# Kernel tuning notes

Hardware: AMD Instinct MI355X
Metric: run time of the kernel (lower is better)

Reference implementation:

```python
import jax, jax.numpy as jnp
import numpy as np

B, T, C, H = 2, 4096, 768, 12
D = C // H  # head_dim = 64


def setup_inputs() -> dict:
    key = jax.random.key(0)
    k1, k2, k3 = jax.random.split(key, 3)
    x = jax.random.normal(k1, (B, T, C), dtype=jnp.float32)
    w_qkv = jax.random.normal(k2, (C, 3 * C), dtype=jnp.float32) * (1.0 / np.sqrt(C))
    w_out = jax.random.normal(k3, (C, C), dtype=jnp.float32) * (1.0 / np.sqrt(C))
    return {"x": x, "w_qkv": w_qkv, "w_out": w_out}


def reference(x, w_qkv, w_out):
    b, t, c = x.shape
    qkv = x @ w_qkv                              # (B,T,3C)
    q, k, v = jnp.split(qkv, 3, axis=-1)
    # (B,T,C) -> (B,H,T,D)
    q = q.reshape(b, t, H, D).transpose(0, 2, 1, 3)
    k = k.reshape(b, t, H, D).transpose(0, 2, 1, 3)
    v = v.reshape(b, t, H, D).transpose(0, 2, 1, 3)
    att = jnp.einsum('bhqd,bhkd->bhqk', q, k) / jnp.sqrt(jnp.float32(D))
    causal = jnp.tril(jnp.ones((t, t), dtype=bool))  # True where allowed
    att = jnp.where(causal, att, -jnp.inf)
    att = jax.nn.softmax(att, axis=-1)
    y = jnp.einsum('bhqk,bhkd->bhqd', att, v)        # (B,H,T,D)
    y = y.transpose(0, 2, 1, 3).reshape(b, t, c)
    return y @ w_out
```

## Files before the change

kernel.cpp:

```cpp
#include <hip/hip_runtime.h>
#include <stdint.h>
#include <stddef.h>

#define NB 2
#define NT 4096
#define NC 768
#define NH 12
#define ND 64

typedef unsigned short u16;
typedef __attribute__((ext_vector_type(2))) float f32x2;
typedef __attribute__((ext_vector_type(4))) float f32x4;
typedef __attribute__((ext_vector_type(16))) float f32x16;
typedef __attribute__((ext_vector_type(8))) unsigned short u16x8;
typedef __attribute__((ext_vector_type(4))) unsigned short u16x4;
typedef __attribute__((ext_vector_type(8))) __bf16 bf16x8;
typedef __attribute__((ext_vector_type(4))) unsigned int u32x4;

typedef __attribute__((address_space(1))) const unsigned int gu32;
typedef __attribute__((address_space(3))) unsigned int lu32;

__device__ __forceinline__ u16 f2bf(float f) {
  uint32_t u = __builtin_bit_cast(uint32_t, f);
  u += 0x7FFFu + ((u >> 16) & 1u);
  return (u16)(u >> 16);
}
__device__ __forceinline__ bf16x8 asbf(u16x8 v) { return __builtin_bit_cast(bf16x8, v); }

__device__ __forceinline__ uint32_t pkbf(float a, float b) {
  uint32_t ua = __builtin_bit_cast(uint32_t, a) + 0x8000u;
  uint32_t ub = __builtin_bit_cast(uint32_t, b) + 0x8000u;
  return __builtin_amdgcn_perm(ub, ua, 0x07060302u);
}
__device__ __forceinline__ uint32_t pktr(float a, float b) {
  return __builtin_amdgcn_perm(__builtin_bit_cast(uint32_t, b),
                               __builtin_bit_cast(uint32_t, a), 0x07060302u);
}

#define GLDS(gsrc, ldst) __builtin_amdgcn_global_load_lds( \
    (gu32*)(gsrc), (lu32*)(ldst), 16, 0, 0)

#define PRE_CAST_BLKS 6144
#define PRE_TA_BX 72
#define PRE_TA_BLKS (72 * 24)
#define PRE_TB_BX 24
#define PRE_TB_BLKS (24 * 24)
__global__ __launch_bounds__(256)
void k_pre(const float* __restrict__ x, u16* __restrict__ xb,
           const float* __restrict__ w_qkv, u16* __restrict__ wqT,
           const float* __restrict__ w_out, u16* __restrict__ woT) {
  __shared__ float tile[32][33];
  const int bid = blockIdx.x;
  const int tid = threadIdx.x;
  if (bid < PRE_CAST_BLKS) {
    int i = bid * 256 + tid;
    f32x4 v = ((const f32x4*)x)[i];
    u16x4 o;
    o[0] = f2bf(v[0]); o[1] = f2bf(v[1]); o[2] = f2bf(v[2]); o[3] = f2bf(v[3]);
    ((u16x4*)xb)[i] = o;
    return;
  }
  const float* in;
  u16* out;
  int R, Cn, bx, by;
  if (bid < PRE_CAST_BLKS + PRE_TA_BLKS) {
    int q = bid - PRE_CAST_BLKS;
    bx = q % PRE_TA_BX; by = q / PRE_TA_BX;
    in = w_qkv; out = wqT; R = NC; Cn = 3 * NC;
  } else {
    int q = bid - PRE_CAST_BLKS - PRE_TA_BLKS;
    bx = q % PRE_TB_BX; by = q / PRE_TB_BX;
    in = w_out; out = woT; R = NC; Cn = NC;
  }
  int c0 = bx * 32, r0 = by * 32;
  int tx = tid & 31, ty = tid >> 5;
  for (int i = ty; i < 32; i += 8)
    tile[i][tx] = in[(size_t)(r0 + i) * Cn + c0 + tx];
  __syncthreads();
  for (int i = ty; i < 32; i += 8)
    out[(size_t)(c0 + i) * R + r0 + tx] = f2bf(tile[tx][i]);
}

template <int EPI, int NBX>
__global__ __launch_bounds__(256, 3)
void k_gemm_bt(const u16* __restrict__ A, const u16* __restrict__ Bt,
               int M, int N, int K,
               u16* __restrict__ o0, u16* __restrict__ o1, u16* __restrict__ o2,
               float* __restrict__ of) {
  __shared__ u16 SMEM[2 * 128 * 64];
  u16* As = SMEM;
  u16* Bs = SMEM + 8192;
  const int tid = threadIdx.x;
  const int wave = tid >> 6, lane = tid & 63, quad = lane >> 4, lc = lane & 15;
  const int wm = (wave & 1) * 64, wn = (wave >> 1) * 64;
  const int wg = blockIdx.x;
  const int nid = (wg & 7) * ((int)gridDim.x >> 3) + (wg >> 3);
  const int bx = nid % NBX, by = nid / NBX;
  const int bm = by * 128, bn = bx * 128;

  const int lr = lane >> 3;
  const int gsw = ((lane & 7) ^ lr) * 8;
  const int rB = wave * 8 + lr;
  const u16* gA = A + (size_t)(bm + rB) * K + gsw;
  const u16* gB = Bt + (size_t)(bn + rB) * K + gsw;
  u16* lA0 = &As[wave * 8 * 64];
  u16* lB0 = &Bs[wave * 8 * 64];

  f32x4 zv = {0.f, 0.f, 0.f, 0.f};
  f32x4 acc[4][4];
#pragma unroll
  for (int i = 0; i < 4; ++i)
#pragma unroll
    for (int j = 0; j < 4; ++j) acc[i][j] = zv;

  for (int k0 = 0; k0 < K; k0 += 64) {
    __syncthreads();
#pragma unroll
    for (int c = 0; c < 4; ++c) {
      GLDS(gA + (size_t)c * 32 * K + k0, lA0 + c * 2048);
      GLDS(gB + (size_t)c * 32 * K + k0, lB0 + c * 2048);
    }
    asm volatile("s_waitcnt vmcnt(0)" ::: "memory");
    __syncthreads();

#pragma unroll
    for (int ks = 0; ks < 2; ++ks) {
      const int ao = (((ks << 2) + quad) ^ (lc & 7)) * 8;
      bf16x8 af[4], bfv[4];
#pragma unroll
      for (int mi = 0; mi < 4; ++mi)
        af[mi] = asbf(*(const u16x8*)&As[(wm + mi * 16 + lc) * 64 + ao]);
#pragma unroll
      for (int ni = 0; ni < 4; ++ni)
        bfv[ni] = asbf(*(const u16x8*)&Bs[(wn + ni * 16 + lc) * 64 + ao]);
#pragma unroll
      for (int mi = 0; mi < 4; ++mi)
#pragma unroll
        for (int ni = 0; ni < 4; ++ni)
          acc[mi][ni] = __builtin_amdgcn_mfma_f32_16x16x32_bf16(af[mi], bfv[ni],
                                                                acc[mi][ni], 0, 0, 0);
    }
  }

  const int sect = (EPI == 1) ? (bn / NC) : 0;
  if (EPI == 1 && sect == 2) {
    const int b = bm >> 12;
    const int tb = bm & (NT - 1);
    const int hb = (bn - 2 * NC) >> 6;
#pragma unroll 1
    for (int r2_ = 0; r2_ < 2; ++r2_) {
      __syncthreads();
      if ((wave >> 1) == r2_) {
#pragma unroll
        for (int mi = 0; mi < 4; ++mi)
#pragma unroll
          for (int ni = 0; ni < 4; ++ni) {
            const int nl = ni * 16 + lc;
#pragma unroll
            for (int r = 0; r < 4; ++r) {
              const int m = wm + mi * 16 + quad * 4 + r;
              SMEM[nl * 128 + (m ^ ((nl & 7) << 3))] = f2bf(acc[mi][ni][r]);
            }
          }
      }
      __syncthreads();
#pragma unroll
      for (int pass = 0; pass < 4; ++pass) {
        const int row = (tid >> 4) + 16 * pass;
        const int chunk = tid & 15;
        u16x8 w = *(const u16x8*)&SMEM[row * 128 + ((chunk ^ (row & 7)) * 8)];
        const int nl = 64 * r2_ + row;
        *(u16x8*)&o2[((size_t)(b * NH + hb + (nl >> 6)) * ND + (nl & 63)) * NT
                     + tb + chunk * 8] = w;
      }
    }
    return;
  }

  const int mrow0 = bm + wm + quad * 4;
#pragma unroll
  for (int mi = 0; mi < 4; ++mi) {
    const int mbase = mrow0 + mi * 16;
#pragma unroll
    for (int ni = 0; ni < 4; ++ni) {
      const int n = bn + wn + ni * 16 + lc;
      if (EPI == 0) {
#pragma unroll
        for (int r = 0; r < 4; ++r)
          of[(size_t)(mbase + r) * N + n] = acc[mi][ni][r];
      } else {
        const int wn2 = n - sect * NC;
        const int h = wn2 >> 6, d = wn2 & 63;
        const int b = mbase >> 12;
        const int t = mbase & (NT - 1);
        const float sc = (sect == 0) ? 0.18033688011112042f : 1.0f;
        u16* dst = (sect == 0) ? o0 : o1;
#pragma unroll
        for (int r = 0; r < 4; ++r)
          dst[((size_t)(b * NH + h) * NT + (t + r)) * ND + d] =
              f2bf(acc[mi][ni][r] * sc);
      }
    }
  }
}

__device__ __forceinline__ void softpack16(const f32x16& s, int qrel, bool msk,
                                           int l5, f32x2& sl2, bf16x8* pf) {
  float e[16];
#pragma unroll
  for (int r = 0; r < 16; ++r) {
    float v = s[r];
    if (msk) {
      int tl = (r & 3) + 8 * (r >> 2) + 4 * l5;
      v = (tl > qrel) ? -1e30f : v;
    }
    e[r] = __builtin_amdgcn_exp2f(v);
  }
  uint32_t wv[8];
#pragma unroll
  for (int i = 0; i < 8; ++i) {
    wv[i] = pktr(e[2 * i], e[2 * i + 1]);
    f32x2 inc = {__builtin_bit_cast(float, wv[i] & 0xFFFF0000u),
                 __builtin_bit_cast(float, wv[i] << 16)};
    sl2 += inc;
  }
#pragma unroll
  for (int g = 0; g < 2; ++g) {
    auto r0 = __builtin_amdgcn_permlane32_swap(wv[g * 4 + 0], wv[g * 4 + 2], false, false);
    auto r1 = __builtin_amdgcn_permlane32_swap(wv[g * 4 + 1], wv[g * 4 + 3], false, false);
    u32x4 f = {r0[0], r1[0], r0[1], r1[1]};
    pf[g] = __builtin_bit_cast(bf16x8, f);
  }
}

__global__ __launch_bounds__(256, 4)
void k_attn(const u16* __restrict__ Q, const u16* __restrict__ K,
            const u16* __restrict__ Vt, u16* __restrict__ Y) {
  __shared__ u16 SM[2][64 * 64];
  __shared__ float PL[2][64];
  const int tid = threadIdx.x;
  const int lane = tid & 63, wave = tid >> 6;
  const int l5 = lane >> 5, l31 = lane & 31;
  const int qh = wave & 1, th = wave >> 1;
  const int bh = blockIdx.x % (NB * NH);
  const int qi = 63 - blockIdx.x / (NB * NH);
  const int b = bh / NH, h = bh - b * NH;
  const u16* __restrict__ Qb = Q + (size_t)bh * NT * ND;
  const u16* __restrict__ Kb = K + (size_t)bh * NT * ND;
  const u16* __restrict__ Vb = Vt + (size_t)bh * (size_t)ND * NT;

  const int qg = qi * 64 + qh * 32 + l31;

  bf16x8 bq[4];
#pragma unroll
  for (int ks = 0; ks < 4; ++ks)
    bq[ks] = asbf(*(const u16x8*)(Qb + (size_t)qg * ND + ks * 16 + l5 * 8));

  f32x16 Zv;
#pragma unroll
  for (int i = 0; i < 16; ++i) Zv[i] = 0.f;
  f32x16 o0 = Zv, o1 = Zv;
  f32x2 sl2 = {0.f, 0.f};

  const int srow = tid >> 3, sg = tid & 7;
  const int soff = srow * 64 + ((sg ^ (srow & 7)) * 8);
  const u16* __restrict__ pK = Kb + (size_t)srow * ND + sg * 8;
  const u16* __restrict__ pV = Vb + (size_t)srow * NT + sg * 8;

  int qfro[4];
#pragma unroll
  for (int ks = 0; ks < 4; ++ks)
    qfro[ks] = (th * 32 + l31) * 64 + (((ks * 2 + l5) ^ (l31 & 7)) * 8);
  int vfro[2];
#pragma unroll
  for (int kp = 0; kp < 2; ++kp)
    vfro[kp] = l31 * 64 + ((((2 * th + kp) * 2 + l5) ^ (l31 & 7)) * 8);

  u16x8 st[4];
  st[0] = *(const u16x8*)(pK);
  st[1] = *(const u16x8*)(pK + (size_t)32 * ND);
  st[2] = *(const u16x8*)(pV);
  st[3] = *(const u16x8*)(pV + (size_t)32 * NT);

#pragma unroll 1
  for (int tau = 0; tau <= qi; ++tau) {
    __syncthreads();
    *(u16x8*)&SM[0][soff] = st[0];
    *(u16x8*)&SM[0][2048 + soff] = st[1];
    *(u16x8*)&SM[1][soff] = st[2];
    *(u16x8*)&SM[1][2048 + soff] = st[3];
    __syncthreads();

    const bool dg = (tau == qi);
    const bool act = !(dg && th > qh);
    bf16x8 p[2];
    if (act) {
      bf16x8 kf0 = asbf(*(const u16x8*)&SM[0][qfro[0]]);
      __builtin_amdgcn_s_setprio(1);
      f32x16 s = __builtin_amdgcn_mfma_f32_32x32x16_bf16(kf0, bq[0], Zv, 0, 0, 0);
#pragma unroll
      for (int ks = 1; ks < 4; ++ks) {
        bf16x8 kf = asbf(*(const u16x8*)&SM[0][qfro[ks]]);
        s = __builtin_amdgcn_mfma_f32_32x32x16_bf16(kf, bq[ks], s, 0, 0, 0);
      }
      __builtin_amdgcn_s_setprio(0);
      softpack16(s, l31, dg && (th == qh), l5, sl2, p);
    }

    if (tau < qi) {
      const int tn = (tau + 1) * 64;
      st[0] = *(const u16x8*)(pK + (size_t)tn * ND);
      st[1] = *(const u16x8*)(pK + (size_t)(tn + 32) * ND);
      st[2] = *(const u16x8*)(pV + tn);
      st[3] = *(const u16x8*)(pV + (size_t)32 * NT + tn);
    }

    if (act) {
      __builtin_amdgcn_s_setprio(1);
#pragma unroll
      for (int kp = 0; kp < 2; ++kp) {
        bf16x8 v0 = asbf(*(const u16x8*)&SM[1][vfro[kp]]);
        bf16x8 v1 = asbf(*(const u16x8*)&SM[1][2048 + vfro[kp]]);
        o0 = __builtin_amdgcn_mfma_f32_32x32x16_bf16(v0, p[kp], o0, 0, 0, 0);
        o1 = __builtin_amdgcn_mfma_f32_32x32x16_bf16(v1, p[kp], o1, 0, 0, 0);
      }
      __builtin_amdgcn_s_setprio(0);
    }
  }

  const float slv = sl2[0] + sl2[1];
  float l = slv + __shfl_xor(slv, 32);
  __syncthreads();
  float* PK = (float*)&SM[0][0];
  if (th == 0) {
#pragma unroll
    for (int r = 0; r < 16; ++r) PK[(qh * 32 + r) * 64 + lane] = o0[r];
#pragma unroll
    for (int r = 0; r < 16; ++r) PK[(qh * 32 + 16 + r) * 64 + lane] = o1[r];
    PL[qh][lane] = l;
  }
  __syncthreads();
  if (th == 1) {
#pragma unroll
    for (int r = 0; r < 16; ++r) o0[r] += PK[(qh * 32 + r) * 64 + lane];
#pragma unroll
    for (int r = 0; r < 16; ++r) o1[r] += PK[(qh * 32 + 16 + r) * 64 + lane];
    l += PL[qh][lane];
    const float inv = 1.f / l;
    u16* yrow = Y + (size_t)(b * NT + qg) * NC + h * 64;
#pragma unroll
    for (int dh = 0; dh < 2; ++dh) {
      const f32x16& o = dh ? o1 : o0;
#pragma unroll
      for (int rq = 0; rq < 4; ++rq) {
        const int d = dh * 32 + 8 * rq + 4 * l5;
        uint2 w;
        w.x = pkbf(o[rq * 4 + 0] * inv, o[rq * 4 + 1] * inv);
        w.y = pkbf(o[rq * 4 + 2] * inv, o[rq * 4 + 3] * inv);
        *(uint2*)&yrow[d] = w;
      }
    }
  }
}

extern "C" void kernel_launch(void* const* d_in, const int* in_sizes, int n_in,
                              void* d_out, int out_size, void* d_ws, size_t ws_size,
                              hipStream_t stream) {
  (void)in_sizes; (void)n_in; (void)out_size; (void)ws_size;
  const float* x = (const float*)d_in[0];
  const float* w_qkv = (const float*)d_in[1];
  const float* w_out = (const float*)d_in[2];
  float* out = (float*)d_out;

  u16* ws = (u16*)d_ws;
  const size_t XE = (size_t)NB * NT * NC;
  u16* xb  = ws;
  u16* wqT = xb + XE;
  u16* woT = wqT + (size_t)3 * NC * NC;
  u16* Qb  = woT + (size_t)NC * NC;
  u16* Kb  = Qb + XE;
  u16* Vtb = Kb + XE;
  u16* yb  = Vtb + XE;

  k_pre<<<dim3(PRE_CAST_BLKS + PRE_TA_BLKS + PRE_TB_BLKS), 256, 0, stream>>>(
      x, xb, w_qkv, wqT, w_out, woT);
  k_gemm_bt<1, 18><<<dim3(18 * 64), 256, 0, stream>>>(
      xb, wqT, NB * NT, 3 * NC, NC, Qb, Kb, Vtb, nullptr);
  k_attn<<<dim3((NB * NH) * 64), 256, 0, stream>>>(Qb, Kb, Vtb, yb);
  k_gemm_bt<0, 6><<<dim3(6 * 64), 256, 0, stream>>>(
      yb, woT, NB * NT, NC, NC, nullptr, nullptr, nullptr, out);
}
```

Measured before the change: 218.6 us.

## Compute softmax row sums via MFMA with ones and retile GEMM block order

The attention kernel now accumulates the softmax denominator with an extra MFMA against a vector of bf16 ones, instead of unpacking the bf16 probabilities and adding them on the VALU. This drops a per-tile cross-lane shuffle-and-sum in exchange for one more matrix instruction per kp step and 16 more accumulator registers, so attention launch bounds are lowered from 4 to 3 waves. Both GEMMs also switch to a supertile ordering (8 M-tiles by 3 N-tiles per group), meant to improve L2 reuse. Because NBX is no longer used, the mapping only covers the grid if N-tiles divide by 3, which holds for 18 and 6.

```diff
diff --git a/kernel.cpp b/kernel.cpp
--- a/kernel.cpp
+++ b/kernel.cpp
@@ -9,7 +9,6 @@
 #define ND 64
 
 typedef unsigned short u16;
-typedef __attribute__((ext_vector_type(2))) float f32x2;
 typedef __attribute__((ext_vector_type(4))) float f32x4;
 typedef __attribute__((ext_vector_type(16))) float f32x16;
 typedef __attribute__((ext_vector_type(8))) unsigned short u16x8;
@@ -81,7 +80,7 @@
     out[(size_t)(c0 + i) * R + r0 + tx] = f2bf(tile[tx][i]);
 }
 
-template <int EPI, int NBX>
+template <int EPI, int NBX, int MT>
 __global__ __launch_bounds__(256, 3)
 void k_gemm_bt(const u16* __restrict__ A, const u16* __restrict__ Bt,
                int M, int N, int K,
@@ -95,7 +94,9 @@
   const int wm = (wave & 1) * 64, wn = (wave >> 1) * 64;
   const int wg = blockIdx.x;
   const int nid = (wg & 7) * ((int)gridDim.x >> 3) + (wg >> 3);
-  const int bx = nid % NBX, by = nid / NBX;
+  const int s = nid / 24, w = nid % 24;
+  const int sm = s % (MT / 8), sn = s / (MT / 8);
+  const int by = sm * 8 + (w & 7), bx = sn * 3 + (w >> 3);
   const int bm = by * 128, bn = bx * 128;
 
   const int lr = lane >> 3;
@@ -168,10 +169,10 @@
       for (int pass = 0; pass < 4; ++pass) {
         const int row = (tid >> 4) + 16 * pass;
         const int chunk = tid & 15;
-        u16x8 w = *(const u16x8*)&SMEM[row * 128 + ((chunk ^ (row & 7)) * 8)];
+        u16x8 wv = *(const u16x8*)&SMEM[row * 128 + ((chunk ^ (row & 7)) * 8)];
         const int nl = 64 * r2_ + row;
         *(u16x8*)&o2[((size_t)(b * NH + hb + (nl >> 6)) * ND + (nl & 63)) * NT
-                     + tb + chunk * 8] = w;
+                     + tb + chunk * 8] = wv;
       }
     }
     return;
@@ -205,7 +206,7 @@
 }
 
 __device__ __forceinline__ void softpack16(const f32x16& s, int qrel, bool msk,
-                                           int l5, f32x2& sl2, bf16x8* pf) {
+                                           int l5, bf16x8* pf) {
   float e[16];
 #pragma unroll
   for (int r = 0; r < 16; ++r) {
@@ -218,12 +219,7 @@
   }
   uint32_t wv[8];
 #pragma unroll
-  for (int i = 0; i < 8; ++i) {
-    wv[i] = pktr(e[2 * i], e[2 * i + 1]);
-    f32x2 inc = {__builtin_bit_cast(float, wv[i] & 0xFFFF0000u),
-                 __builtin_bit_cast(float, wv[i] << 16)};
-    sl2 += inc;
-  }
+  for (int i = 0; i < 8; ++i) wv[i] = pktr(e[2 * i], e[2 * i + 1]);
 #pragma unroll
   for (int g = 0; g < 2; ++g) {
     auto r0 = __builtin_amdgcn_permlane32_swap(wv[g * 4 + 0], wv[g * 4 + 2], false, false);
@@ -233,7 +229,7 @@
   }
 }
 
-__global__ __launch_bounds__(256, 4)
+__global__ __launch_bounds__(256, 3)
 void k_attn(const u16* __restrict__ Q, const u16* __restrict__ K,
             const u16* __restrict__ Vt, u16* __restrict__ Y) {
   __shared__ u16 SM[2][64 * 64];
@@ -256,11 +252,16 @@
   for (int ks = 0; ks < 4; ++ks)
     bq[ks] = asbf(*(const u16x8*)(Qb + (size_t)qg * ND + ks * 16 + l5 * 8));
 
+  u16x8 onesu;
+#pragma unroll
+  for (int i = 0; i < 8; ++i) onesu[i] = (u16)0x3F80;
+  const bf16x8 ones = asbf(onesu);
+
   f32x16 Zv;
 #pragma unroll
   for (int i = 0; i < 16; ++i) Zv[i] = 0.f;
   f32x16 o0 = Zv, o1 = Zv;
-  f32x2 sl2 = {0.f, 0.f};
+  f32x16 lacc = Zv;
 
   const int srow = tid >> 3, sg = tid & 7;
   const int soff = srow * 64 + ((sg ^ (srow & 7)) * 8);
@@ -304,7 +305,7 @@
         s = __builtin_amdgcn_mfma_f32_32x32x16_bf16(kf, bq[ks], s, 0, 0, 0);
       }
       __builtin_amdgcn_s_setprio(0);
-      softpack16(s, l31, dg && (th == qh), l5, sl2, p);
+      softpack16(s, l31, dg && (th == qh), l5, p);
     }
 
     if (tau < qi) {
@@ -323,13 +324,13 @@
         bf16x8 v1 = asbf(*(const u16x8*)&SM[1][2048 + vfro[kp]]);
         o0 = __builtin_amdgcn_mfma_f32_32x32x16_bf16(v0, p[kp], o0, 0, 0, 0);
         o1 = __builtin_amdgcn_mfma_f32_32x32x16_bf16(v1, p[kp], o1, 0, 0, 0);
+        lacc = __builtin_amdgcn_mfma_f32_32x32x16_bf16(ones, p[kp], lacc, 0, 0, 0);
       }
       __builtin_amdgcn_s_setprio(0);
     }
   }
 
-  const float slv = sl2[0] + sl2[1];
-  float l = slv + __shfl_xor(slv, 32);
+  float l = lacc[0];
   __syncthreads();
   float* PK = (float*)&SM[0][0];
   if (th == 0) {
@@ -384,9 +385,9 @@
 
   k_pre<<<dim3(PRE_CAST_BLKS + PRE_TA_BLKS + PRE_TB_BLKS), 256, 0, stream>>>(
       x, xb, w_qkv, wqT, w_out, woT);
-  k_gemm_bt<1, 18><<<dim3(18 * 64), 256, 0, stream>>>(
+  k_gemm_bt<1, 18, 64><<<dim3(18 * 64), 256, 0, stream>>>(
       xb, wqT, NB * NT, 3 * NC, NC, Qb, Kb, Vtb, nullptr);
   k_attn<<<dim3((NB * NH) * 64), 256, 0, stream>>>(Qb, Kb, Vtb, yb);
-  k_gemm_bt<0, 6><<<dim3(6 * 64), 256, 0, stream>>>(
+  k_gemm_bt<0, 6, 64><<<dim3(6 * 64), 256, 0, stream>>>(
       yb, woT, NB * NT, NC, NC, nullptr, nullptr, nullptr, out);
 }
```

Measured after the change: 214.4 us. Within noise of the previous version (-1.9%).
